# Optimization experiments

Hardware: AMD Instinct MI355X
Metric: run time of the kernel (lower is better)

The kernel has to match this reference:

```python
import jax, jax.numpy as jnp
import numpy as np

DIM = 1024
N_HEADS = 16
D_K = DIM // N_HEADS
B, N = 2, 2048


def _pairwise_dist(p):
    # p: [B, N, 3] -> Euclidean cdist [B, N, N], grad-safe at zero distance
    sq = jnp.sum(p * p, axis=-1)                      # [B, N]
    d2 = sq[:, :, None] + sq[:, None, :] - 2.0 * jnp.einsum('bnd,bmd->bnm', p, p)
    d2 = jnp.maximum(d2, 0.0)
    safe = jnp.where(d2 > 0.0, d2, 1.0)
    return jnp.where(d2 > 0.0, jnp.sqrt(safe), 0.0)


def setup_inputs() -> dict:
    key = jax.random.key(0)
    ks = jax.random.split(key, 11)
    s = 1.0 / np.sqrt(DIM)
    inp = {
        'x': jax.random.normal(ks[0], (B, N, DIM), jnp.float32),
        'positions': jax.random.normal(ks[1], (B, N, 3), jnp.float32),
        'W_q': jax.random.normal(ks[2], (DIM, DIM), jnp.float32) * s,
        'b_q': jnp.zeros((DIM,), jnp.float32),
        'W_k': jax.random.normal(ks[3], (DIM, DIM), jnp.float32) * s,
        'b_k': jnp.zeros((DIM,), jnp.float32),
        'W_v': jax.random.normal(ks[4], (DIM, DIM), jnp.float32) * s,
        'b_v': jnp.zeros((DIM,), jnp.float32),
        'W_o': jax.random.normal(ks[5], (DIM, DIM), jnp.float32) * s,
        'b_o': jnp.zeros((DIM,), jnp.float32),
        'dist_bias': jax.random.normal(ks[6], (N_HEADS, 1, 1), jnp.float32),
    }
    return inp


def reference(x, positions, W_q, b_q, W_k, b_k, W_v, b_v, W_o, b_o, dist_bias):
    Bv, Nv, C = x.shape
    def proj(W, b):
        # [B,N,C] -> [B,H,N,d_k]
        return (x @ W.T + b).reshape(Bv, Nv, N_HEADS, D_K).transpose(0, 2, 1, 3)
    Q = proj(W_q, b_q)
    K = proj(W_k, b_k)
    V = proj(W_v, b_v)
    attn = jnp.einsum('bhnd,bhmd->bhnm', Q, K) / np.sqrt(D_K)  # [B,H,N,N]
    dists = _pairwise_dist(positions)                          # [B,N,N]
    # log(exp(-|b|*d) + 1e-8), per-head bias broadcast over [B,H,N,N]
    dist_weights = jnp.exp(-jnp.abs(dist_bias)[None] * dists[:, None])
    attn = attn + jnp.log(dist_weights + 1e-8)
    attn = jax.nn.softmax(attn, axis=-1)
    out = jnp.einsum('bhnm,bhmd->bhnd', attn, V)               # [B,H,N,d_k]
    out = out.transpose(0, 2, 1, 3).reshape(Bv, Nv, C)
    return out @ W_o.T + b_o
```

## Files before the change

### kernel.cpp

```cpp
#include <hip/hip_runtime.h>
#include <hip/hip_bf16.h>
#include <stdint.h>

using bf16   = __hip_bfloat16;
using short8 = __attribute__((ext_vector_type(8))) short;
using f32x4  = __attribute__((ext_vector_type(4))) float;
using f32x16 = __attribute__((ext_vector_type(16))) float;

#define NSEQ   2048
#define NHEADS 16
#define DK     64
#define DMODEL 1024

#define GLDS16(gp, lp) __builtin_amdgcn_global_load_lds( \
    (const __attribute__((address_space(1))) void*)(gp), \
    (__attribute__((address_space(3))) void*)(lp), 16, 0, 0)

__device__ __forceinline__ ushort f2bf(float f){
  bf16 h = __float2bfloat16(f);
  return __builtin_bit_cast(ushort, h);
}
__device__ __forceinline__ float bf2f(ushort u){
  uint t = ((uint)u)<<16; return __builtin_bit_cast(float, t);
}

__global__ void k_cvt(const float4* __restrict__ src, ushort4* __restrict__ dst, int n4){
  int i = blockIdx.x*blockDim.x + threadIdx.x;
  if (i >= n4) return;
  float4 v = src[i];
  ushort4 o;
  o.x = f2bf(v.x); o.y = f2bf(v.y); o.z = f2bf(v.z); o.w = f2bf(v.w);
  dst[i] = o;
}

__global__ void k_geo(const float* __restrict__ pos, ushort* __restrict__ AF,
                      ushort* __restrict__ BF, int n){
  int i = blockIdx.x*blockDim.x + threadIdx.x;
  if (i >= n) return;
  float x = pos[i*3+0], y = pos[i*3+1], z = pos[i*3+2];
  float sq = x*x + y*y + z*z;
  ushort xh = f2bf(x);  float xhf = bf2f(xh);  ushort xl = f2bf(x - xhf);
  ushort yh = f2bf(y);  float yhf = bf2f(yh);  ushort yl = f2bf(y - yhf);
  ushort zh = f2bf(z);  float zhf = bf2f(zh);  ushort zl = f2bf(z - zhf);
  ushort sh = f2bf(sq); float shf = bf2f(sh);  ushort sl = f2bf(sq - shf);
  ushort m2xh = f2bf(-2.f*xhf), m2xl = f2bf(-2.f*bf2f(xl));
  ushort m2yh = f2bf(-2.f*yhf), m2yl = f2bf(-2.f*bf2f(yl));
  ushort m2zh = f2bf(-2.f*zhf), m2zl = f2bf(-2.f*bf2f(zl));
  const ushort one = 0x3F80;
  ushort af[16] = {xh,xl,xh, yh,yl,yh, zh,zl,zh, sh,sl, one,one, 0,0,0};
  ushort bv[16] = {m2xh,m2xh,m2xl, m2yh,m2yh,m2yl, m2zh,m2zh,m2zl, one,one, sh,sl, 0,0,0};
  *(uint4*)&AF[i*16]     = *(uint4*)&af[0];
  *(uint4*)&AF[i*16 + 8] = *(uint4*)&af[8];
  *(uint4*)&BF[i*16]     = *(uint4*)&bv[0];
  *(uint4*)&BF[i*16 + 8] = *(uint4*)&bv[8];
}

__device__ __forceinline__ void gemm_core(
    const ushort* __restrict__ Ap, const ushort* __restrict__ Bp,
    int bm, int bn, int tid, ushort smem[2][2][4096], f32x4 (&acc)[4][4])
{
  const int wave = tid>>6, lane = tid&63;
  const int wr = wave>>1, wc = wave&1;
  const int ko   = (lane>>4)*8;
  const int srow = wave*16 + (lane>>2);
  const int scol = (lane&3)*8;

  const ushort* As = Ap + (size_t)(bm*128)*DMODEL + scol;
  const ushort* Bs = Bp + (size_t)(bn*128)*DMODEL + scol;

#define STAGE(buf, kt) do { \
    _Pragma("unroll") \
    for (int i_=0;i_<2;i_++){ \
      GLDS16(As + (size_t)(i_*64 + srow)*DMODEL + (kt)*32, &smem[buf][0][i_*2048 + wave*512]); \
      GLDS16(Bs + (size_t)(i_*64 + srow)*DMODEL + (kt)*32, &smem[buf][1][i_*2048 + wave*512]); \
    } } while(0)

  STAGE(0, 0);
  for (int kt=0; kt<32; ++kt){
    int cur = kt&1;
    __syncthreads();
    if (kt<31) STAGE(cur^1, kt+1);
    short8 af[4], bfv[4];
    const ushort* At = smem[cur][0];
    const ushort* Bt = smem[cur][1];
    #pragma unroll
    for (int mi=0;mi<4;mi++) af[mi]  = *(const short8*)&At[(wr*64+mi*16+(lane&15))*32 + ko];
    #pragma unroll
    for (int ni=0;ni<4;ni++) bfv[ni] = *(const short8*)&Bt[(wc*64+ni*16+(lane&15))*32 + ko];
    #pragma unroll
    for (int mi=0;mi<4;mi++)
      #pragma unroll
      for (int ni=0;ni<4;ni++)
        acc[mi][ni] = __builtin_amdgcn_mfma_f32_16x16x32_bf16(af[mi], bfv[ni], acc[mi][ni], 0,0,0);
  }
#undef STAGE
}

__global__ __launch_bounds__(256) void k_gemm_qkv(
    const ushort* __restrict__ xb,
    const ushort* __restrict__ Wqb, const ushort* __restrict__ Wkb, const ushort* __restrict__ Wvb,
    const float* __restrict__ bq, const float* __restrict__ bk, const float* __restrict__ bv,
    ushort* __restrict__ Qo, ushort* __restrict__ Ko, ushort* __restrict__ Vto)
{
  __shared__ ushort smem[2][2][4096];
  const int tid = threadIdx.x;
  const int t = blockIdx.x & 255;
  const int z = blockIdx.x >> 8;
  const int lane = tid&63, wave = tid>>6;
  const int wr = wave>>1, wc = wave&1;

  const ushort* Ap; const ushort* Bp; const float* bias;
  ushort* outp; int bm, bn; float scale = 1.0f;
  if (z==0){ Ap=xb;  Bp=Wqb; bias=bq; outp=Qo;  bm=t>>3; bn=t&7; scale=0.125f; }
  else if (z==1){ Ap=xb;  Bp=Wkb; bias=bk; outp=Ko;  bm=t>>3; bn=t&7; }
  else          { Ap=Wvb; Bp=xb;  bias=bv; outp=Vto; bm=t&7;  bn=t>>3; }

  f32x4 acc[4][4] = {};
  gemm_core(Ap, Bp, bm, bn, tid, smem, acc);

  if (z<2){
    #pragma unroll
    for (int mi=0;mi<4;mi++){
      const int m0 = bm*128 + wr*64 + mi*16 + (lane>>4)*4;
      #pragma unroll
      for (int ni=0;ni<4;ni++){
        const int nn = bn*128 + wc*64 + ni*16 + (lane&15);
        const float bs = bias[nn];
        const int h = nn>>6, d = nn&63;
        #pragma unroll
        for (int j=0;j<4;j++){
          int mm = m0+j;
          int b = mm>>11, nr = mm&2047;
          size_t off = (((size_t)(b*NHEADS+h)*NSEQ) + nr)*DK + d;
          outp[off] = f2bf((acc[mi][ni][j] + bs)*scale);
        }
      }
    }
  } else {
    #pragma unroll
    for (int mi=0;mi<4;mi++){
      const int m0 = bm*128 + wr*64 + mi*16 + (lane>>4)*4;
      #pragma unroll
      for (int ni=0;ni<4;ni++){
        const int nn = bn*128 + wc*64 + ni*16 + (lane&15);
        const int b = nn>>11, nr = nn&2047;
        #pragma unroll
        for (int j=0;j<4;j++){
          int mm = m0+j;
          const float bs = bias[mm];
          int h = mm>>6, d = mm&63;
          size_t off = (((size_t)(b*NHEADS+h)*DK) + d)*NSEQ + nr;
          outp[off] = f2bf(acc[mi][ni][j] + bs);
        }
      }
    }
  }
}

__global__ __launch_bounds__(256) void k_gemm_out(
    const ushort* __restrict__ Ob, const ushort* __restrict__ Wob,
    const float* __restrict__ bo, float* __restrict__ out)
{
  __shared__ ushort smem[2][2][4096];
  const int tid = threadIdx.x;
  const int t = blockIdx.x;
  const int lane = tid&63, wave = tid>>6;
  const int wr = wave>>1, wc = wave&1;
  const int bm = t>>3, bn = t&7;
  f32x4 acc[4][4] = {};
  gemm_core(Ob, Wob, bm, bn, tid, smem, acc);
  #pragma unroll
  for (int mi=0;mi<4;mi++){
    const int m0 = bm*128 + wr*64 + mi*16 + (lane>>4)*4;
    #pragma unroll
    for (int ni=0;ni<4;ni++){
      const int nn = bn*128 + wc*64 + ni*16 + (lane&15);
      const float bs = bo[nn];
      #pragma unroll
      for (int j=0;j<4;j++)
        out[(size_t)(m0+j)*DMODEL + nn] = acc[mi][ni][j] + bs;
    }
  }
}

__global__ __launch_bounds__(128) void k_attn(
    const ushort* __restrict__ Q, const ushort* __restrict__ K, const ushort* __restrict__ Vt,
    const ushort* __restrict__ AF, const ushort* __restrict__ BF,
    const float* __restrict__ dist_bias,
    ushort* __restrict__ op0, ushort* __restrict__ op1, float* __restrict__ lpart)
{
  const int tid = threadIdx.x, wave = tid>>6, lane = tid&63;
  const int qt = blockIdx.x, h = blockIdx.y, z = blockIdx.z;
  const int b = z>>1, c = z&1;
  const int lo5 = lane&31, hi = lane>>5;
  const float ah = fabsf(dist_bias[h]);
  const ushort* Qh  = Q  + ((size_t)(b*NHEADS+h))*NSEQ*DK;
  const ushort* Kh  = K  + ((size_t)(b*NHEADS+h))*NSEQ*DK;
  const ushort* Vth = Vt + ((size_t)(b*NHEADS+h))*DK*NSEQ;
  const ushort* AFb = AF + (size_t)b*NSEQ*16;
  const ushort* BFb = BF + (size_t)b*NSEQ*16;

  const int q0 = qt*64 + wave*32;

  short8 qf[4];
  #pragma unroll
  for (int s=0;s<4;s++)
    qf[s] = *(const short8*)&Qh[(size_t)(q0+lo5)*DK + s*16 + hi*8];
  const short8 bfq = *(const short8*)&BFb[(size_t)(q0+lo5)*16 + hi*8];

  f32x16 o0 = {}, o1 = {};
  float l_run = 0.f;
  const int j0 = c*1024;

  for (int jt=0; jt<32; ++jt){
    const int jb = j0 + jt*32;
    const short8 afk = *(const short8*)&AFb[(size_t)(jb+lo5)*16 + hi*8];
    f32x16 zz = {};
    f32x16 d2 = __builtin_amdgcn_mfma_f32_32x32x16_bf16(afk, bfq, zz, 0,0,0);
    f32x16 st = {};
    #pragma unroll
    for (int s=0;s<4;s++){
      short8 kf = *(const short8*)&Kh[(size_t)(jb+lo5)*DK + s*16 + hi*8];
      st = __builtin_amdgcn_mfma_f32_32x32x16_bf16(kf, qf[s], st, 0,0,0);
    }
    const short8 v00 = *(const short8*)&Vth[(size_t)(lo5)*NSEQ      + jb      + hi*8];
    const short8 v01 = *(const short8*)&Vth[(size_t)(lo5)*NSEQ      + jb + 16 + hi*8];
    const short8 v10 = *(const short8*)&Vth[(size_t)(32+lo5)*NSEQ   + jb      + hi*8];
    const short8 v11 = *(const short8*)&Vth[(size_t)(32+lo5)*NSEQ   + jb + 16 + hi*8];
    float p[16];
    #pragma unroll
    for (int r=0;r<16;r++){
      float d = __builtin_amdgcn_sqrtf(fmaxf(d2[r], 0.f));
      p[r] = __expf(fmaf(-ah, d, st[r]));
    }
    float s01=p[0]+p[1], s23=p[2]+p[3], s45=p[4]+p[5], s67=p[6]+p[7];
    float s89=p[8]+p[9], sab=p[10]+p[11], scd=p[12]+p[13], sef=p[14]+p[15];
    float t0=s01+s23, t1=s45+s67, t2=s89+sab, t3=scd+sef;
    float rsum = (t0+t1)+(t2+t3);
    rsum += __shfl_xor(rsum, 32);
    l_run += rsum;
    #pragma unroll
    for (int s=0;s<2;s++){
      uint w0, w1, w2, w3;
      asm("v_cvt_pk_bf16_f32 %0, %1, %2" : "=v"(w0) : "v"(p[8*s+0]), "v"(p[8*s+1]));
      asm("v_cvt_pk_bf16_f32 %0, %1, %2" : "=v"(w2) : "v"(p[8*s+4]), "v"(p[8*s+5]));
      asm("v_cvt_pk_bf16_f32 %0, %1, %2" : "=v"(w1) : "v"(p[8*s+2]), "v"(p[8*s+3]));
      asm("v_cvt_pk_bf16_f32 %0, %1, %2" : "=v"(w3) : "v"(p[8*s+6]), "v"(p[8*s+7]));
      asm volatile("v_permlane32_swap_b32 %0, %1" : "+v"(w0), "+v"(w2));
      asm volatile("v_permlane32_swap_b32 %0, %1" : "+v"(w1), "+v"(w3));
      uint4 aw; aw.x = w0; aw.y = w1; aw.z = w2; aw.w = w3;
      const short8 pa = __builtin_bit_cast(short8, aw);
      if (s==0){
        o0 = __builtin_amdgcn_mfma_f32_32x32x16_bf16(pa, v00, o0, 0,0,0);
        o1 = __builtin_amdgcn_mfma_f32_32x32x16_bf16(pa, v10, o1, 0,0,0);
      } else {
        o0 = __builtin_amdgcn_mfma_f32_32x32x16_bf16(pa, v01, o0, 0,0,0);
        o1 = __builtin_amdgcn_mfma_f32_32x32x16_bf16(pa, v11, o1, 0,0,0);
      }
    }
  }
  ushort* op = (c ? op1 : op0) + ((size_t)(b*NHEADS+h))*NSEQ*DK;
  #pragma unroll
  for (int r=0;r<16;r++){
    const int qr = q0 + (r&3) + 8*(r>>2) + 4*hi;
    op[(size_t)qr*DK + lo5]      = f2bf(o0[r]);
    op[(size_t)qr*DK + 32 + lo5] = f2bf(o1[r]);
  }
  if (hi==0)
    lpart[(size_t)c*(2*NHEADS*NSEQ) + (size_t)(b*NHEADS+h)*NSEQ + q0 + lo5] = l_run;
}

__global__ void k_merge(const ushort* __restrict__ op0, const ushort* __restrict__ op1,
                        const float* __restrict__ lpart, ushort* __restrict__ Ob){
  const int idx = blockIdx.x*blockDim.x + threadIdx.x;
  const int row = idx>>3, dg = idx&7;
  const int q = row & 2047, bh = row >> 11;
  const int b = bh >> 4, h = bh & 15;
  const size_t po = (size_t)row*64 + dg*8;
  const short8 a  = *(const short8*)&op0[po];
  const short8 b8 = *(const short8*)&op1[po];
  const float inv = 1.f/(lpart[row] + lpart[65536 + row]);
  ushort o[8];
  #pragma unroll
  for (int j=0;j<8;j++)
    o[j] = f2bf((bf2f((ushort)a[j]) + bf2f((ushort)b8[j]))*inv);
  *(short8*)&Ob[((size_t)b*NSEQ + q)*DMODEL + h*DK + dg*8] = *(short8*)&o[0];
}

extern "C" void kernel_launch(void* const* d_in, const int* in_sizes, int n_in,
                              void* d_out, int out_size, void* d_ws, size_t ws_size,
                              hipStream_t stream) {
  const float* x   = (const float*)d_in[0];
  const float* pos = (const float*)d_in[1];
  const float* Wq  = (const float*)d_in[2];
  const float* bq  = (const float*)d_in[3];
  const float* Wk  = (const float*)d_in[4];
  const float* bk  = (const float*)d_in[5];
  const float* Wv  = (const float*)d_in[6];
  const float* bv  = (const float*)d_in[7];
  const float* Wo  = (const float*)d_in[8];
  const float* bo  = (const float*)d_in[9];
  const float* db  = (const float*)d_in[10];
  float* out = (float*)d_out;

  char* ws = (char*)d_ws;
  ushort* xb   = (ushort*)(ws);
  ushort* Wqb  = (ushort*)(ws + ((size_t)8<<20));
  ushort* Wkb  = (ushort*)(ws + ((size_t)10<<20));
  ushort* Wvb  = (ushort*)(ws + ((size_t)12<<20));
  ushort* Wob  = (ushort*)(ws + ((size_t)14<<20));
  ushort* Qb   = (ushort*)(ws + ((size_t)16<<20));
  ushort* Kb   = (ushort*)(ws + ((size_t)24<<20));
  ushort* Vtb  = (ushort*)(ws + ((size_t)32<<20));
  ushort* op1  = (ushort*)(ws + ((size_t)40<<20));
  ushort* op0  = xb;
  ushort* AFt  = Wqb;
  ushort* BFt  = (ushort*)(ws + ((size_t)8<<20) + (128<<10));
  float*  lpart= (float*) (ws + ((size_t)8<<20) + (256<<10));
  ushort* Omrg = Qb;

  k_cvt<<<4096, 256, 0, stream>>>((const float4*)x,  (ushort4*)xb,  1048576);
  k_cvt<<<1024, 256, 0, stream>>>((const float4*)Wq, (ushort4*)Wqb, 262144);
  k_cvt<<<1024, 256, 0, stream>>>((const float4*)Wk, (ushort4*)Wkb, 262144);
  k_cvt<<<1024, 256, 0, stream>>>((const float4*)Wv, (ushort4*)Wvb, 262144);
  k_cvt<<<1024, 256, 0, stream>>>((const float4*)Wo, (ushort4*)Wob, 262144);
  k_gemm_qkv<<<768, 256, 0, stream>>>(xb, Wqb, Wkb, Wvb, bq, bk, bv, Qb, Kb, Vtb);
  k_geo<<<16, 256, 0, stream>>>(pos, AFt, BFt, 2*NSEQ);
  k_attn<<<dim3(32,NHEADS,4), 128, 0, stream>>>(Qb, Kb, Vtb, AFt, BFt, db, op0, op1, lpart);
  k_merge<<<2048, 256, 0, stream>>>(op0, op1, lpart, Omrg);
  k_gemm_out<<<256, 256, 0, stream>>>(Omrg, Wob, bo, out);
}
```

Before: 290.6 us.

## Split KV across waves within block and reduce in LDS, drop merge kernel

The attention kernel no longer splits the key range across two grid-level chunks with a separate merge kernel. Each block now covers 32 queries with 4 waves, each wave handling a quarter of the keys. The partial outputs and row sums are reduced through shared memory, then normalized and written directly in the layout the output GEMM expects. This removes the partial-output round trip through global memory and one kernel launch. In exchange it adds LDS traffic, three block barriers, and a reduction tail in which only one wave writes.

```diff
diff --git a/kernel.cpp b/kernel.cpp
--- a/kernel.cpp
+++ b/kernel.cpp
@@ -183,15 +183,16 @@
   }
 }
 
-__global__ __launch_bounds__(128) void k_attn(
+__global__ __launch_bounds__(256) void k_attn(
     const ushort* __restrict__ Q, const ushort* __restrict__ K, const ushort* __restrict__ Vt,
     const ushort* __restrict__ AF, const ushort* __restrict__ BF,
     const float* __restrict__ dist_bias,
-    ushort* __restrict__ op0, ushort* __restrict__ op1, float* __restrict__ lpart)
+    ushort* __restrict__ O)
 {
+  __shared__ float red[2][2048];
+  __shared__ float lred[4][32];
   const int tid = threadIdx.x, wave = tid>>6, lane = tid&63;
-  const int qt = blockIdx.x, h = blockIdx.y, z = blockIdx.z;
-  const int b = z>>1, c = z&1;
+  const int qt = blockIdx.x, h = blockIdx.y, b = blockIdx.z;
   const int lo5 = lane&31, hi = lane>>5;
   const float ah = fabsf(dist_bias[h]);
   const ushort* Qh  = Q  + ((size_t)(b*NHEADS+h))*NSEQ*DK;
@@ -200,7 +201,7 @@
   const ushort* AFb = AF + (size_t)b*NSEQ*16;
   const ushort* BFb = BF + (size_t)b*NSEQ*16;
 
-  const int q0 = qt*64 + wave*32;
+  const int q0 = qt*32;
 
   short8 qf[4];
   #pragma unroll
@@ -210,9 +211,9 @@
 
   f32x16 o0 = {}, o1 = {};
   float l_run = 0.f;
-  const int j0 = c*1024;
-
-  for (int jt=0; jt<32; ++jt){
+  const int j0 = wave*512;
+
+  for (int jt=0; jt<16; ++jt){
     const int jb = j0 + jt*32;
     const short8 afk = *(const short8*)&AFb[(size_t)(jb+lo5)*16 + hi*8];
     f32x16 zz = {};
@@ -235,8 +236,7 @@
     }
     float s01=p[0]+p[1], s23=p[2]+p[3], s45=p[4]+p[5], s67=p[6]+p[7];
     float s89=p[8]+p[9], sab=p[10]+p[11], scd=p[12]+p[13], sef=p[14]+p[15];
-    float t0=s01+s23, t1=s45+s67, t2=s89+sab, t3=scd+sef;
-    float rsum = (t0+t1)+(t2+t3);
+    float rsum = ((s01+s23)+(s45+s67)) + ((s89+sab)+(scd+sef));
     rsum += __shfl_xor(rsum, 32);
     l_run += rsum;
     #pragma unroll
@@ -259,32 +259,49 @@
       }
     }
   }
-  ushort* op = (c ? op1 : op0) + ((size_t)(b*NHEADS+h))*NSEQ*DK;
-  #pragma unroll
-  for (int r=0;r<16;r++){
-    const int qr = q0 + (r&3) + 8*(r>>2) + 4*hi;
-    op[(size_t)qr*DK + lo5]      = f2bf(o0[r]);
-    op[(size_t)qr*DK + 32 + lo5] = f2bf(o1[r]);
-  }
-  if (hi==0)
-    lpart[(size_t)c*(2*NHEADS*NSEQ) + (size_t)(b*NHEADS+h)*NSEQ + q0 + lo5] = l_run;
-}
-
-__global__ void k_merge(const ushort* __restrict__ op0, const ushort* __restrict__ op1,
-                        const float* __restrict__ lpart, ushort* __restrict__ Ob){
-  const int idx = blockIdx.x*blockDim.x + threadIdx.x;
-  const int row = idx>>3, dg = idx&7;
-  const int q = row & 2047, bh = row >> 11;
-  const int b = bh >> 4, h = bh & 15;
-  const size_t po = (size_t)row*64 + dg*8;
-  const short8 a  = *(const short8*)&op0[po];
-  const short8 b8 = *(const short8*)&op1[po];
-  const float inv = 1.f/(lpart[row] + lpart[65536 + row]);
-  ushort o[8];
-  #pragma unroll
-  for (int j=0;j<8;j++)
-    o[j] = f2bf((bf2f((ushort)a[j]) + bf2f((ushort)b8[j]))*inv);
-  *(short8*)&Ob[((size_t)b*NSEQ + q)*DMODEL + h*DK + dg*8] = *(short8*)&o[0];
+
+#define STORE_ACC(buf) do { \
+    float* rb = red[buf]; \
+    _Pragma("unroll") \
+    for (int g=0; g<8; ++g){ \
+      const int sl = (g + lane) & 7; \
+      float4 t; \
+      if (g<4){ t.x=o0[g*4]; t.y=o0[g*4+1]; t.z=o0[g*4+2]; t.w=o0[g*4+3]; } \
+      else    { t.x=o1[(g-4)*4]; t.y=o1[(g-4)*4+1]; t.z=o1[(g-4)*4+2]; t.w=o1[(g-4)*4+3]; } \
+      *(float4*)&rb[lane*32 + sl*4] = t; \
+    } } while(0)
+#define LOAD_ADD_ACC(buf) do { \
+    const float* rb = red[buf]; \
+    _Pragma("unroll") \
+    for (int g=0; g<8; ++g){ \
+      const int sl = (g + lane) & 7; \
+      float4 t = *(const float4*)&rb[lane*32 + sl*4]; \
+      if (g<4){ o0[g*4]+=t.x; o0[g*4+1]+=t.y; o0[g*4+2]+=t.z; o0[g*4+3]+=t.w; } \
+      else    { o1[(g-4)*4]+=t.x; o1[(g-4)*4+1]+=t.y; o1[(g-4)*4+2]+=t.z; o1[(g-4)*4+3]+=t.w; } \
+    } } while(0)
+
+  if (wave >= 2) STORE_ACC(wave-2);
+  if (wave != 0 && hi == 0) lred[wave][lo5] = l_run;
+  __syncthreads();
+  if (wave < 2) LOAD_ADD_ACC(wave);
+  __syncthreads();
+  if (wave == 1) STORE_ACC(0);
+  __syncthreads();
+  if (wave == 0){
+    LOAD_ADD_ACC(0);
+    l_run += lred[1][lo5] + lred[2][lo5] + lred[3][lo5];
+    #pragma unroll
+    for (int r=0;r<16;r++){
+      const int src = (r&3) + 8*(r>>2) + 4*hi;
+      const float lr = __shfl(l_run, src);
+      const float inv = 1.f/lr;
+      const int i = q0 + src;
+      O[((size_t)b*NSEQ + i)*DMODEL + h*DK + lo5]      = f2bf(o0[r]*inv);
+      O[((size_t)b*NSEQ + i)*DMODEL + h*DK + 32 + lo5] = f2bf(o1[r]*inv);
+    }
+  }
+#undef STORE_ACC
+#undef LOAD_ADD_ACC
 }
 
 extern "C" void kernel_launch(void* const* d_in, const int* in_sizes, int n_in,
@@ -312,12 +329,9 @@
   ushort* Qb   = (ushort*)(ws + ((size_t)16<<20));
   ushort* Kb   = (ushort*)(ws + ((size_t)24<<20));
   ushort* Vtb  = (ushort*)(ws + ((size_t)32<<20));
-  ushort* op1  = (ushort*)(ws + ((size_t)40<<20));
-  ushort* op0  = xb;
   ushort* AFt  = Wqb;
   ushort* BFt  = (ushort*)(ws + ((size_t)8<<20) + (128<<10));
-  float*  lpart= (float*) (ws + ((size_t)8<<20) + (256<<10));
-  ushort* Omrg = Qb;
+  ushort* Omrg = xb;
 
   k_cvt<<<4096, 256, 0, stream>>>((const float4*)x,  (ushort4*)xb,  1048576);
   k_cvt<<<1024, 256, 0, stream>>>((const float4*)Wq, (ushort4*)Wqb, 262144);
@@ -326,7 +340,6 @@
   k_cvt<<<1024, 256, 0, stream>>>((const float4*)Wo, (ushort4*)Wob, 262144);
   k_gemm_qkv<<<768, 256, 0, stream>>>(xb, Wqb, Wkb, Wvb, bq, bk, bv, Qb, Kb, Vtb);
   k_geo<<<16, 256, 0, stream>>>(pos, AFt, BFt, 2*NSEQ);
-  k_attn<<<dim3(32,NHEADS,4), 128, 0, stream>>>(Qb, Kb, Vtb, AFt, BFt, db, op0, op1, lpart);
-  k_merge<<<2048, 256, 0, stream>>>(op0, op1, lpart, Omrg);
+  k_attn<<<dim3(64,NHEADS,2), 256, 0, stream>>>(Qb, Kb, Vtb, AFt, BFt, db, Omrg);
   k_gemm_out<<<256, 256, 0, stream>>>(Omrg, Wob, bo, out);
 }
```

New measurement: 294.2 us. About the same (+1.2%).
